# Optimization experiments

Hardware: AMD Instinct MI355X
Metric: run time of the kernel (lower is better)

Reference implementation:

```python
import jax, jax.numpy as jnp
import numpy as np

B, C, D, M = 256, 1024, 512, 4096
EPS = 1e-12  # F.normalize default eps


def setup_inputs() -> dict:
    key = jax.random.key(0)
    k1, k2 = jax.random.split(key)
    feature = jax.random.normal(k1, (B, C, D), dtype=jnp.float32)
    memory = jax.random.normal(k2, (M, C), dtype=jnp.float32)
    mask = jnp.ones((B,), dtype=bool)
    return {"feature": feature, "memory": memory, "mask": mask, "train": 1}


def reference(feature, memory, mask, train):
    # ---- Global_Pattern_Adjustment ----
    attn = jax.nn.softmax(feature.mean(axis=1), axis=-1)            # [B, D]
    feature_G = (feature * attn[:, None, :]).mean(axis=-1)          # [B, C]
    score = feature_G @ memory.T                                    # [B, M]
    score_memory = jax.nn.softmax(score, axis=0)                    # softmax over batch
    score_image = jax.nn.softmax(score, axis=1)                     # softmax over memory slots
    memory_response = jax.lax.stop_gradient(score_image) @ memory   # [B, C]
    memory_response = feature_G + memory_response
    global_compensation = feature + memory_response[:, :, None]     # [B, C, D]

    if not train:
        return global_compensation

    # ---- Memory_Evolution (mask-filtered rows emulated by zeroing their update) ----
    idx = jnp.argmax(score_image, axis=1)                           # topk(k=1) -> [B]
    weights = jnp.take_along_axis(score_memory, idx[:, None], axis=1)  # [B, 1]
    m = mask.astype(feature.dtype)[:, None]                         # [B, 1]
    update_vector = feature_G * weights * m                         # [B, C]
    increment = jnp.zeros_like(memory).at[idx].add(update_vector)   # scatter_add -> [M, C]
    upd = increment + memory
    norm = jnp.maximum(jnp.linalg.norm(upd, axis=1, keepdims=True), EPS)
    updated_memory = jax.lax.stop_gradient(upd / norm)              # [M, C]
    return (global_compensation, updated_memory)
```

## Files before the change

kernel.cpp:

```cpp
#include <hip/hip_runtime.h>
#include <math.h>

#define B 256
#define C 1024
#define D 512
#define M 4096
#define KS_SC 4
#define KS_MR 8
#define CHUNK 64
#define CPB 32
#define NCP (C / CPB)
static constexpr float EPS = 1e-12f;

typedef float fx4 __attribute__((ext_vector_type(4)));
typedef short bf16x8 __attribute__((ext_vector_type(8)));
typedef float f32x4 __attribute__((ext_vector_type(4)));

static __device__ __forceinline__ unsigned short f2bf(float x) {
    unsigned u = __builtin_bit_cast(unsigned, x);
    return (unsigned short)((u + 0x7fffu + ((u >> 16) & 1u)) >> 16);
}

__global__ __launch_bounds__(256) void k_convmem(const float* __restrict__ mem,
                                                 unsigned short* __restrict__ memB,
                                                 unsigned short* __restrict__ memBT) {
    __shared__ unsigned short lds[64][65];
    int tm = blockIdx.x * 64;
    int tc = blockIdx.y * 64;
    int t = threadIdx.x;
    int rr = t >> 4, c4 = t & 15;
#pragma unroll
    for (int i = 0; i < 4; ++i) {
        int row = rr + 16 * i;
        float4 v = *reinterpret_cast<const float4*>(mem + (size_t)(tm + row) * C + tc + c4 * 4);
        unsigned short b0 = f2bf(v.x), b1 = f2bf(v.y), b2 = f2bf(v.z), b3 = f2bf(v.w);
        ushort4 w = make_ushort4(b0, b1, b2, b3);
        *reinterpret_cast<ushort4*>(memB + (size_t)(tm + row) * C + tc + c4 * 4) = w;
        lds[row][c4 * 4 + 0] = b0; lds[row][c4 * 4 + 1] = b1;
        lds[row][c4 * 4 + 2] = b2; lds[row][c4 * 4 + 3] = b3;
    }
    __syncthreads();
#pragma unroll
    for (int i = 0; i < 4; ++i) {
        int colC = rr + 16 * i;
        ushort4 w = make_ushort4(lds[c4 * 4 + 0][colC], lds[c4 * 4 + 1][colC],
                                 lds[c4 * 4 + 2][colC], lds[c4 * 4 + 3][colC]);
        *reinterpret_cast<ushort4*>(memBT + (size_t)(tc + colC) * M + tm + c4 * 4) = w;
    }
}

__global__ __launch_bounds__(256) void k_colmean(const float* __restrict__ f,
                                                 float* __restrict__ colpart, int b0) {
    __shared__ fx4 buf[128];
    int bx = blockIdx.x, cc = blockIdx.y;
    int b = b0 + bx;
    int t = threadIdx.x;
    int r = t >> 7, lane = t & 127;
    const fx4* f4 = reinterpret_cast<const fx4*>(f)
                  + ((size_t)b * C + cc * CPB + r * 16) * (D / 4) + lane;
    fx4 acc = (fx4)(0.f);
#pragma unroll
    for (int k = 0; k < 16; ++k) acc += f4[(size_t)k * (D / 4)];
    if (r) buf[lane] = acc;
    __syncthreads();
    if (!r) {
        acc += buf[lane];
        reinterpret_cast<fx4*>(colpart)[((size_t)cc * CHUNK + bx) * (D / 4) + lane] = acc;
    }
}

__global__ __launch_bounds__(256) void k_attn(const float* __restrict__ colpart,
                                              float* __restrict__ attnD, int b0) {
    __shared__ float red[256];
    int bl = blockIdx.x;
    int b = b0 + bl;
    int t = threadIdx.x;
    float s0 = 0.f, s1 = 0.f;
#pragma unroll
    for (int p = 0; p < NCP; ++p) {
        s0 += colpart[((size_t)p * CHUNK + bl) * D + t];
        s1 += colpart[((size_t)p * CHUNK + bl) * D + t + 256];
    }
    float x0 = s0 * (1.0f / C), x1 = s1 * (1.0f / C);
    red[t] = fmaxf(x0, x1); __syncthreads();
    for (int s = 128; s > 0; s >>= 1) {
        if (t < s) red[t] = fmaxf(red[t], red[t + s]);
        __syncthreads();
    }
    float mx = red[0]; __syncthreads();
    float e0 = expf(x0 - mx), e1 = expf(x1 - mx);
    red[t] = e0 + e1; __syncthreads();
    for (int s = 128; s > 0; s >>= 1) {
        if (t < s) red[t] += red[t + s];
        __syncthreads();
    }
    float inv = 1.0f / (red[0] * (float)D);
    attnD[(size_t)b * D + t] = e0 * inv;
    attnD[(size_t)b * D + t + 256] = e1 * inv;
}

__global__ __launch_bounds__(256) void k_fg(const float* __restrict__ f,
                                            const float* __restrict__ attnD,
                                            float* __restrict__ fG,
                                            unsigned short* __restrict__ fGB, int b0) {
    int w = blockIdx.x * 4 + (threadIdx.x >> 6);
    int lane = threadIdx.x & 63;
    int b = b0 + (w >> 10);
    int c = w & 1023;
    const float4* f4 = reinterpret_cast<const float4*>(f) + ((size_t)b * C + c) * (D / 4);
    const float4* a4 = reinterpret_cast<const float4*>(attnD) + (size_t)b * (D / 4);
    float4 v0 = f4[lane], v1 = f4[lane + 64];
    float4 a0 = a4[lane], a1 = a4[lane + 64];
    float acc = v0.x * a0.x + v0.y * a0.y + v0.z * a0.z + v0.w * a0.w
              + v1.x * a1.x + v1.y * a1.y + v1.z * a1.z + v1.w * a1.w;
    for (int s = 32; s > 0; s >>= 1) acc += __shfl_xor(acc, s, 64);
    if (lane == 0) {
        fG[(size_t)b * C + c] = acc;
        fGB[(size_t)b * C + c] = f2bf(acc);
    }
}

__global__ __launch_bounds__(256) void k_score(const unsigned short* __restrict__ fGB,
                                               const unsigned short* __restrict__ memB,
                                               float* __restrict__ score_p) {
    int t = threadIdx.x;
    int lane = t & 63, wid = t >> 6;
    int wm = wid >> 1, wn = wid & 1;
    int brow = blockIdx.y * 64 + wm * 32;
    int mcol = blockIdx.x * 64 + wn * 32;
    int kc0 = blockIdx.z * (C / KS_SC);
    int l16 = lane & 15, kg = lane >> 4;
    f32x4 acc00 = {}, acc01 = {}, acc10 = {}, acc11 = {};
#pragma unroll
    for (int ks = 0; ks < C / KS_SC / 32; ++ks) {
        int kb = kc0 + ks * 32 + kg * 8;
        bf16x8 a0 = *reinterpret_cast<const bf16x8*>(fGB + (size_t)(brow + l16) * C + kb);
        bf16x8 a1 = *reinterpret_cast<const bf16x8*>(fGB + (size_t)(brow + 16 + l16) * C + kb);
        bf16x8 b0 = *reinterpret_cast<const bf16x8*>(memB + (size_t)(mcol + l16) * C + kb);
        bf16x8 b1 = *reinterpret_cast<const bf16x8*>(memB + (size_t)(mcol + 16 + l16) * C + kb);
        acc00 = __builtin_amdgcn_mfma_f32_16x16x32_bf16(a0, b0, acc00, 0, 0, 0);
        acc01 = __builtin_amdgcn_mfma_f32_16x16x32_bf16(a0, b1, acc01, 0, 0, 0);
        acc10 = __builtin_amdgcn_mfma_f32_16x16x32_bf16(a1, b0, acc10, 0, 0, 0);
        acc11 = __builtin_amdgcn_mfma_f32_16x16x32_bf16(a1, b1, acc11, 0, 0, 0);
    }
    float* o = score_p + (size_t)blockIdx.z * B * M;
#pragma unroll
    for (int r = 0; r < 4; ++r) {
        int row0 = brow + kg * 4 + r, row1 = row0 + 16;
        o[(size_t)row0 * M + mcol + l16]      = acc00[r];
        o[(size_t)row0 * M + mcol + 16 + l16] = acc01[r];
        o[(size_t)row1 * M + mcol + l16]      = acc10[r];
        o[(size_t)row1 * M + mcol + 16 + l16] = acc11[r];
    }
}

__global__ __launch_bounds__(1024) void k_rowsoftmax(const float* __restrict__ score_p,
                                                     float* __restrict__ scoreF,
                                                     unsigned short* __restrict__ simgB,
                                                     int* __restrict__ idxout,
                                                     float* __restrict__ rowinv) {
    __shared__ float srow[M];
    __shared__ float rv[1024];
    __shared__ int ri[1024];
    int b = blockIdx.x, t = threadIdx.x;
    const float* p = score_p + (size_t)b * M;
    float mx = -INFINITY; int mi = 0;
    for (int j = t; j < M; j += 1024) {
        float s = p[j] + p[j + (size_t)B * M] + p[j + 2 * (size_t)B * M]
                + p[j + 3 * (size_t)B * M];
        srow[j] = s;
        scoreF[(size_t)b * M + j] = s;
        if (s > mx) { mx = s; mi = j; }
    }
    rv[t] = mx; ri[t] = mi; __syncthreads();
    for (int s = 512; s > 0; s >>= 1) {
        if (t < s) {
            if (rv[t + s] > rv[t] || (rv[t + s] == rv[t] && ri[t + s] < ri[t])) {
                rv[t] = rv[t + s]; ri[t] = ri[t + s];
            }
        }
        __syncthreads();
    }
    float rmax = rv[0]; int rid = ri[0];
    __syncthreads();
    float s = 0.f;
    for (int j = t; j < M; j += 1024) {
        float e = expf(srow[j] - rmax);
        simgB[(size_t)b * M + j] = f2bf(e);
        s += e;
    }
    rv[t] = s; __syncthreads();
    for (int ss = 512; ss > 0; ss >>= 1) {
        if (t < ss) rv[t] += rv[t + ss];
        __syncthreads();
    }
    if (t == 0) { idxout[b] = rid; rowinv[b] = 1.0f / rv[0]; }
}

__global__ __launch_bounds__(256) void k_mr(const unsigned short* __restrict__ simgB,
                                            const unsigned short* __restrict__ memBT,
                                            float* __restrict__ mr_p) {
    int t = threadIdx.x;
    int lane = t & 63, wid = t >> 6;
    int wm = wid >> 1, wn = wid & 1;
    int brow = blockIdx.y * 64 + wm * 32;
    int ccol = blockIdx.x * 64 + wn * 32;
    int kc0 = blockIdx.z * (M / KS_MR);
    int l16 = lane & 15, kg = lane >> 4;
    f32x4 acc00 = {}, acc01 = {}, acc10 = {}, acc11 = {};
#pragma unroll 4
    for (int ks = 0; ks < M / KS_MR / 32; ++ks) {
        int kb = kc0 + ks * 32 + kg * 8;
        bf16x8 a0 = *reinterpret_cast<const bf16x8*>(simgB + (size_t)(brow + l16) * M + kb);
        bf16x8 a1 = *reinterpret_cast<const bf16x8*>(simgB + (size_t)(brow + 16 + l16) * M + kb);
        bf16x8 b0 = *reinterpret_cast<const bf16x8*>(memBT + (size_t)(ccol + l16) * M + kb);
        bf16x8 b1 = *reinterpret_cast<const bf16x8*>(memBT + (size_t)(ccol + 16 + l16) * M + kb);
        acc00 = __builtin_amdgcn_mfma_f32_16x16x32_bf16(a0, b0, acc00, 0, 0, 0);
        acc01 = __builtin_amdgcn_mfma_f32_16x16x32_bf16(a0, b1, acc01, 0, 0, 0);
        acc10 = __builtin_amdgcn_mfma_f32_16x16x32_bf16(a1, b0, acc10, 0, 0, 0);
        acc11 = __builtin_amdgcn_mfma_f32_16x16x32_bf16(a1, b1, acc11, 0, 0, 0);
    }
    float* o = mr_p + (size_t)blockIdx.z * B * C;
#pragma unroll
    for (int r = 0; r < 4; ++r) {
        int row0 = brow + kg * 4 + r, row1 = row0 + 16;
        o[(size_t)row0 * C + ccol + l16]      = acc00[r];
        o[(size_t)row0 * C + ccol + 16 + l16] = acc01[r];
        o[(size_t)row1 * C + ccol + l16]      = acc10[r];
        o[(size_t)row1 * C + ccol + 16 + l16] = acc11[r];
    }
}

__global__ __launch_bounds__(256) void k_mrred(const float* __restrict__ mr_p,
                                               const float* __restrict__ fG,
                                               const float* __restrict__ rowinv,
                                               float* __restrict__ mrf) {
    size_t row = (size_t)blockIdx.x * 256 + threadIdx.x;
    float a = 0.f;
#pragma unroll
    for (int z = 0; z < KS_MR; ++z) a += mr_p[(size_t)z * B * C + row];
    mrf[row] = fG[row] + rowinv[row >> 10] * a;
}

__global__ __launch_bounds__(256) void k_out(const float* __restrict__ f,
                                             const float* __restrict__ mrf,
                                             float* __restrict__ out) {
    size_t n4 = (size_t)B * C * D / 4;
    const fx4* f4 = reinterpret_cast<const fx4*>(f);
    fx4* o4 = reinterpret_cast<fx4*>(out);
    for (size_t i = (size_t)blockIdx.x * blockDim.x + threadIdx.x; i < n4;
         i += (size_t)gridDim.x * blockDim.x) {
        size_t row = (size_t)B * C - 1 - (i >> 7);
        size_t j = i & 127;
        size_t o = row * 128 + j;
        fx4 v = f4[o];
        v += mrf[row];
        __builtin_nontemporal_store(v, o4 + o);
    }
}

__global__ __launch_bounds__(256) void k_memupd(const float* __restrict__ mem,
                                                const float* __restrict__ fG,
                                                const int* __restrict__ idx,
                                                const float* __restrict__ scoreF,
                                                float* __restrict__ out2) {
    int m = blockIdx.x, t = threadIdx.x;
    __shared__ int sIdx[B];
    __shared__ float se[B];
    __shared__ float red[256];
    __shared__ int sAny;
    if (t == 0) sAny = 0;
    __syncthreads();
    sIdx[t] = idx[t];
    __syncthreads();
    if (sIdx[t] == m) sAny = 1;
    __syncthreads();

    const fx4* m4 = reinterpret_cast<const fx4*>(mem) + (size_t)m * (C / 4);
    fx4 u = m4[t];
    if (sAny) {
        float x = scoreF[(size_t)t * M + m];
        red[t] = x; __syncthreads();
        for (int s = 128; s > 0; s >>= 1) {
            if (t < s) red[t] = fmaxf(red[t], red[t + s]);
            __syncthreads();
        }
        float mx = red[0]; __syncthreads();
        float e = expf(x - mx);
        se[t] = e;
        red[t] = e; __syncthreads();
        for (int s = 128; s > 0; s >>= 1) {
            if (t < s) red[t] += red[t + s];
            __syncthreads();
        }
        float Sinv = 1.0f / red[0];
        __syncthreads();
        for (int b2 = 0; b2 < B; ++b2) {
            if (sIdx[b2] == m) {
                float w = se[b2] * Sinv;
                fx4 g = reinterpret_cast<const fx4*>(fG)[(size_t)b2 * (C / 4) + t];
                u += g * w;
            }
        }
    }
    red[t] = u.x * u.x + u.y * u.y + u.z * u.z + u.w * u.w;
    __syncthreads();
    for (int s = 128; s > 0; s >>= 1) {
        if (t < s) red[t] += red[t + s];
        __syncthreads();
    }
    float invn = 1.0f / fmaxf(sqrtf(red[0]), EPS);
    reinterpret_cast<fx4*>(out2)[(size_t)m * (C / 4) + t] = u * invn;
}

extern "C" void kernel_launch(void* const* d_in, const int* in_sizes, int n_in,
                              void* d_out, int out_size, void* d_ws, size_t ws_size,
                              hipStream_t stream) {
    const float* feature = (const float*)d_in[0];
    const float* memory  = (const float*)d_in[1];
    float* out = (float*)d_out;

    float* ws = (float*)d_ws;
    float* colpart = ws;
    float* attnD   = colpart + (size_t)NCP * CHUNK * D;
    float* fG      = attnD + (size_t)B * D;
    float* scoreF  = fG + (size_t)B * C;
    float* score_p = scoreF + (size_t)B * M;
    float* mr_p    = score_p + (size_t)KS_SC * B * M;
    float* mrf     = mr_p + (size_t)KS_MR * B * C;
    float* rowinv  = mrf + (size_t)B * C;
    int*   idx     = (int*)(rowinv + B);
    unsigned short* fGB   = (unsigned short*)(idx + B);
    unsigned short* memB  = fGB + (size_t)B * C;
    unsigned short* memBT = memB + (size_t)M * C;
    unsigned short* simgB = memBT + (size_t)C * M;

    k_convmem<<<dim3(M / 64, C / 64), 256, 0, stream>>>(memory, memB, memBT);
    for (int b0 = 0; b0 < B; b0 += CHUNK) {
        k_colmean<<<dim3(CHUNK, NCP), 256, 0, stream>>>(feature, colpart, b0);
        k_attn<<<CHUNK, 256, 0, stream>>>(colpart, attnD, b0);
        k_fg<<<CHUNK * C / 4, 256, 0, stream>>>(feature, attnD, fG, fGB, b0);
    }
    k_score<<<dim3(M / 64, B / 64, KS_SC), 256, 0, stream>>>(fGB, memB, score_p);
    k_rowsoftmax<<<B, 1024, 0, stream>>>(score_p, scoreF, simgB, idx, rowinv);
    k_mr<<<dim3(C / 64, B / 64, KS_MR), 256, 0, stream>>>(simgB, memBT, mr_p);
    k_mrred<<<B * C / 256, 256, 0, stream>>>(mr_p, fG, rowinv, mrf);
    k_out<<<4096, 256, 0, stream>>>(feature, mrf, out);
    k_memupd<<<M, 256, 0, stream>>>(memory, fG, idx, scoreF, out + (size_t)B * C * D);
}
```

Baseline: 498.7 us.

## Fuse attention softmax and split-K reduction via last-block atomic counters

Removes the separate k_attn and k_mrred launches. Each uses a last-arriving-block pattern with atomic counters, reset in k_convmem, so the final block of each group does the reduction. The colpart buffer is enlarged to cover all batches, so chunks no longer reuse it. This saves five kernel launches and their inter-kernel gaps, at the cost of threadfences and a serialized tail in the last block of each group.

```diff
diff --git a/kernel.cpp b/kernel.cpp
--- a/kernel.cpp
+++ b/kernel.cpp
@@ -23,11 +23,17 @@
 
 __global__ __launch_bounds__(256) void k_convmem(const float* __restrict__ mem,
                                                  unsigned short* __restrict__ memB,
-                                                 unsigned short* __restrict__ memBT) {
+                                                 unsigned short* __restrict__ memBT,
+                                                 int* __restrict__ cntA,
+                                                 int* __restrict__ cntM) {
     __shared__ unsigned short lds[64][65];
+    int t = threadIdx.x;
+    if (blockIdx.x == 0 && blockIdx.y == 0) {
+        cntA[t] = 0;
+        if (t < 64) cntM[t] = 0;
+    }
     int tm = blockIdx.x * 64;
     int tc = blockIdx.y * 64;
-    int t = threadIdx.x;
     int rr = t >> 4, c4 = t & 15;
 #pragma unroll
     for (int i = 0; i < 4; ++i) {
@@ -50,8 +56,12 @@
 }
 
 __global__ __launch_bounds__(256) void k_colmean(const float* __restrict__ f,
-                                                 float* __restrict__ colpart, int b0) {
+                                                 float* __restrict__ colpart,
+                                                 float* __restrict__ attnD,
+                                                 int* __restrict__ cntA, int b0) {
     __shared__ fx4 buf[128];
+    __shared__ float red[256];
+    __shared__ int sflag;
     int bx = blockIdx.x, cc = blockIdx.y;
     int b = b0 + bx;
     int t = threadIdx.x;
@@ -65,38 +75,37 @@
     __syncthreads();
     if (!r) {
         acc += buf[lane];
-        reinterpret_cast<fx4*>(colpart)[((size_t)cc * CHUNK + bx) * (D / 4) + lane] = acc;
-    }
-}
-
-__global__ __launch_bounds__(256) void k_attn(const float* __restrict__ colpart,
-                                              float* __restrict__ attnD, int b0) {
-    __shared__ float red[256];
-    int bl = blockIdx.x;
-    int b = b0 + bl;
-    int t = threadIdx.x;
-    float s0 = 0.f, s1 = 0.f;
-#pragma unroll
-    for (int p = 0; p < NCP; ++p) {
-        s0 += colpart[((size_t)p * CHUNK + bl) * D + t];
-        s1 += colpart[((size_t)p * CHUNK + bl) * D + t + 256];
-    }
-    float x0 = s0 * (1.0f / C), x1 = s1 * (1.0f / C);
-    red[t] = fmaxf(x0, x1); __syncthreads();
-    for (int s = 128; s > 0; s >>= 1) {
-        if (t < s) red[t] = fmaxf(red[t], red[t + s]);
-        __syncthreads();
-    }
-    float mx = red[0]; __syncthreads();
-    float e0 = expf(x0 - mx), e1 = expf(x1 - mx);
-    red[t] = e0 + e1; __syncthreads();
-    for (int s = 128; s > 0; s >>= 1) {
-        if (t < s) red[t] += red[t + s];
-        __syncthreads();
-    }
-    float inv = 1.0f / (red[0] * (float)D);
-    attnD[(size_t)b * D + t] = e0 * inv;
-    attnD[(size_t)b * D + t + 256] = e1 * inv;
+        reinterpret_cast<fx4*>(colpart)[((size_t)cc * B + b) * (D / 4) + lane] = acc;
+    }
+    __threadfence();
+    __syncthreads();
+    if (t == 0) sflag = (atomicAdd(&cntA[b], 1) == NCP - 1);
+    __syncthreads();
+    if (sflag) {
+        __threadfence();
+        float s0 = 0.f, s1 = 0.f;
+#pragma unroll
+        for (int p = 0; p < NCP; ++p) {
+            s0 += colpart[((size_t)p * B + b) * D + t];
+            s1 += colpart[((size_t)p * B + b) * D + t + 256];
+        }
+        float x0 = s0 * (1.0f / C), x1 = s1 * (1.0f / C);
+        red[t] = fmaxf(x0, x1); __syncthreads();
+        for (int s = 128; s > 0; s >>= 1) {
+            if (t < s) red[t] = fmaxf(red[t], red[t + s]);
+            __syncthreads();
+        }
+        float mx = red[0]; __syncthreads();
+        float e0 = expf(x0 - mx), e1 = expf(x1 - mx);
+        red[t] = e0 + e1; __syncthreads();
+        for (int s = 128; s > 0; s >>= 1) {
+            if (t < s) red[t] += red[t + s];
+            __syncthreads();
+        }
+        float inv = 1.0f / (red[0] * (float)D);
+        attnD[(size_t)b * D + t] = e0 * inv;
+        attnD[(size_t)b * D + t + 256] = e1 * inv;
+    }
 }
 
 __global__ __launch_bounds__(256) void k_fg(const float* __restrict__ f,
@@ -199,12 +208,18 @@
 
 __global__ __launch_bounds__(256) void k_mr(const unsigned short* __restrict__ simgB,
                                             const unsigned short* __restrict__ memBT,
-                                            float* __restrict__ mr_p) {
+                                            const float* __restrict__ fG,
+                                            const float* __restrict__ rowinv,
+                                            float* __restrict__ mr_p,
+                                            float* __restrict__ mrf,
+                                            int* __restrict__ cntM) {
+    __shared__ int sflag;
     int t = threadIdx.x;
     int lane = t & 63, wid = t >> 6;
     int wm = wid >> 1, wn = wid & 1;
-    int brow = blockIdx.y * 64 + wm * 32;
-    int ccol = blockIdx.x * 64 + wn * 32;
+    int br0 = blockIdx.y * 64, cc0 = blockIdx.x * 64;
+    int brow = br0 + wm * 32;
+    int ccol = cc0 + wn * 32;
     int kc0 = blockIdx.z * (M / KS_MR);
     int l16 = lane & 15, kg = lane >> 4;
     f32x4 acc00 = {}, acc01 = {}, acc10 = {}, acc11 = {};
@@ -229,17 +244,30 @@
         o[(size_t)row1 * C + ccol + l16]      = acc10[r];
         o[(size_t)row1 * C + ccol + 16 + l16] = acc11[r];
     }
-}
-
-__global__ __launch_bounds__(256) void k_mrred(const float* __restrict__ mr_p,
-                                               const float* __restrict__ fG,
-                                               const float* __restrict__ rowinv,
-                                               float* __restrict__ mrf) {
-    size_t row = (size_t)blockIdx.x * 256 + threadIdx.x;
-    float a = 0.f;
-#pragma unroll
-    for (int z = 0; z < KS_MR; ++z) a += mr_p[(size_t)z * B * C + row];
-    mrf[row] = fG[row] + rowinv[row >> 10] * a;
+    int tile = blockIdx.y * gridDim.x + blockIdx.x;
+    __threadfence();
+    __syncthreads();
+    if (t == 0) sflag = (atomicAdd(&cntM[tile], 1) == KS_MR - 1);
+    __syncthreads();
+    if (sflag) {
+        __threadfence();
+        int row = t >> 2;
+        int gr = br0 + row;
+        float rinv = rowinv[gr];
+#pragma unroll
+        for (int q = 0; q < 4; ++q) {
+            int gc = cc0 + (t & 3) * 16 + q * 4;
+            float4 a = *reinterpret_cast<const float4*>(fG + (size_t)gr * C + gc);
+#pragma unroll
+            for (int z = 0; z < KS_MR; ++z) {
+                float4 v = *reinterpret_cast<const float4*>(
+                    mr_p + (size_t)z * B * C + (size_t)gr * C + gc);
+                a.x += rinv * v.x; a.y += rinv * v.y;
+                a.z += rinv * v.z; a.w += rinv * v.w;
+            }
+            *reinterpret_cast<float4*>(mrf + (size_t)gr * C + gc) = a;
+        }
+    }
 }
 
 __global__ __launch_bounds__(256) void k_out(const float* __restrict__ f,
@@ -322,7 +350,7 @@
 
     float* ws = (float*)d_ws;
     float* colpart = ws;
-    float* attnD   = colpart + (size_t)NCP * CHUNK * D;
+    float* attnD   = colpart + (size_t)NCP * B * D;
     float* fG      = attnD + (size_t)B * D;
     float* scoreF  = fG + (size_t)B * C;
     float* score_p = scoreF + (size_t)B * M;
@@ -330,21 +358,22 @@
     float* mrf     = mr_p + (size_t)KS_MR * B * C;
     float* rowinv  = mrf + (size_t)B * C;
     int*   idx     = (int*)(rowinv + B);
-    unsigned short* fGB   = (unsigned short*)(idx + B);
+    int*   cntA    = idx + B;
+    int*   cntM    = cntA + B;
+    unsigned short* fGB   = (unsigned short*)(cntM + 64);
     unsigned short* memB  = fGB + (size_t)B * C;
     unsigned short* memBT = memB + (size_t)M * C;
     unsigned short* simgB = memBT + (size_t)C * M;
 
-    k_convmem<<<dim3(M / 64, C / 64), 256, 0, stream>>>(memory, memB, memBT);
+    k_convmem<<<dim3(M / 64, C / 64), 256, 0, stream>>>(memory, memB, memBT, cntA, cntM);
     for (int b0 = 0; b0 < B; b0 += CHUNK) {
-        k_colmean<<<dim3(CHUNK, NCP), 256, 0, stream>>>(feature, colpart, b0);
-        k_attn<<<CHUNK, 256, 0, stream>>>(colpart, attnD, b0);
+        k_colmean<<<dim3(CHUNK, NCP), 256, 0, stream>>>(feature, colpart, attnD, cntA, b0);
         k_fg<<<CHUNK * C / 4, 256, 0, stream>>>(feature, attnD, fG, fGB, b0);
     }
     k_score<<<dim3(M / 64, B / 64, KS_SC), 256, 0, stream>>>(fGB, memB, score_p);
     k_rowsoftmax<<<B, 1024, 0, stream>>>(score_p, scoreF, simgB, idx, rowinv);
-    k_mr<<<dim3(C / 64, B / 64, KS_MR), 256, 0, stream>>>(simgB, memBT, mr_p);
-    k_mrred<<<B * C / 256, 256, 0, stream>>>(mr_p, fG, rowinv, mrf);
+    k_mr<<<dim3(C / 64, B / 64, KS_MR), 256, 0, stream>>>(simgB, memBT, fG, rowinv,
+                                                          mr_p, mrf, cntM);
     k_out<<<4096, 256, 0, stream>>>(feature, mrf, out);
     k_memupd<<<M, 256, 0, stream>>>(memory, fG, idx, scoreF, out + (size_t)B * C * D);
 }
```

Measured after the change: 1.971 ms. 3.95x slower.
